# Kernel tuning notes

Hardware: AMD Instinct MI355X
Metric: run time of the kernel (lower is better)

The kernel has to match this reference:

```python
import jax, jax.numpy as jnp
import numpy as np

N_NODES = 100000
N_EDGES = 1600000
IN_CH, HID_CH, N_CLASS = 512, 128, 40


def setup_inputs() -> dict:
    key = jax.random.key(0)
    k1, k2, k3, k4 = jax.random.split(key, 4)
    x = jax.random.normal(k1, (N_NODES, IN_CH), dtype=jnp.float32)
    edge_index = jax.random.randint(k2, (2, N_EDGES), 0, N_NODES, dtype=jnp.int64)
    W1 = jax.random.normal(k3, (IN_CH, HID_CH), dtype=jnp.float32) * (1.0 / np.sqrt(IN_CH))
    b1 = jnp.zeros((HID_CH,), dtype=jnp.float32)
    W2 = jax.random.normal(k4, (HID_CH, N_CLASS), dtype=jnp.float32) * (1.0 / np.sqrt(HID_CH))
    b2 = jnp.zeros((N_CLASS,), dtype=jnp.float32)
    return {"x": x, "edge_index": edge_index, "W1": W1, "b1": b1, "W2": W2, "b2": b2}


def _gcn_conv(x, src, dst, norm, W, b, n_nodes):
    # transform then sparse normalized aggregation: out = D^-1/2 (A+I) D^-1/2 (x W) + b
    h = x @ W                                  # [N, out_ch]
    msg = h[src] * norm[:, None]               # gather + scale, [E+N, out_ch]
    return jax.ops.segment_sum(msg, dst, num_segments=n_nodes) + b


def reference(x, edge_index, W1, b1, W2, b2):
    n = x.shape[0]
    loop = jnp.arange(n, dtype=edge_index.dtype)
    src = jnp.concatenate([edge_index[0], loop])   # add self-loops
    dst = jnp.concatenate([edge_index[1], loop])
    deg = jax.ops.segment_sum(jnp.ones_like(src, dtype=x.dtype), dst, num_segments=n)
    dinv = jnp.where(deg > 0, jax.lax.rsqrt(deg), 0.0)
    norm = dinv[src] * dinv[dst]                   # symmetric normalization

    h = jax.nn.relu(_gcn_conv(x, src, dst, norm, W1, b1, n))
    # dropout(p=0.5, train=False) -> identity in eval mode
    logits = _gcn_conv(h, src, dst, norm, W2, b2, n)
    return jax.nn.log_softmax(logits, axis=1)
```

## Files before the change

### kernel.cpp

```cpp
#include <hip/hip_runtime.h>
#include <math.h>

#define IN_CH 512
#define HID 128
#define NCLASS 40
#define SCAN_CHUNK 2048
#define FILL_CHUNKS 2048

typedef __attribute__((ext_vector_type(8))) short short8;
typedef __attribute__((ext_vector_type(4))) float float4v;

static __device__ inline ushort f2bf(float f) {
    unsigned int u = __float_as_uint(f);
    u += 0x7fffu + ((u >> 16) & 1u);
    return (ushort)(u >> 16);
}
static __device__ inline float bf2f(ushort u) {
    return __uint_as_float(((unsigned int)u) << 16);
}

__global__ void k_count(const int* __restrict__ dst, int E, int* __restrict__ cnt) {
    int i = blockIdx.x * blockDim.x + threadIdx.x;
    if (i < E) atomicAdd(&cnt[dst[i]], 1);
}

__global__ void k_dinv(const int* __restrict__ cnt, float* __restrict__ dinv, int n) {
    int i = blockIdx.x * blockDim.x + threadIdx.x;
    if (i < n) dinv[i] = rsqrtf((float)cnt[i] + 1.0f);
}

__global__ __launch_bounds__(256) void k_scan_local(const int* __restrict__ cnt,
                                                    int* __restrict__ rowptr,
                                                    int* __restrict__ blocksum, int n) {
    __shared__ int ssum[256];
    int b = blockIdx.x, t = threadIdx.x;
    int base = b * SCAN_CHUNK + t * 8;
    int v[8], s = 0;
    #pragma unroll
    for (int i = 0; i < 8; ++i) {
        int idx = base + i;
        v[i] = (idx < n) ? cnt[idx] : 0;
        s += v[i];
    }
    ssum[t] = s;
    __syncthreads();
    for (int off = 1; off < 256; off <<= 1) {
        int x = (t >= off) ? ssum[t - off] : 0;
        __syncthreads();
        ssum[t] += x;
        __syncthreads();
    }
    int run = ssum[t] - s;
    #pragma unroll
    for (int i = 0; i < 8; ++i) {
        int idx = base + i;
        if (idx < n) rowptr[idx] = run;
        run += v[i];
    }
    if (t == 255) blocksum[b] = ssum[255];
}

__global__ void k_scan_blocksums(int* blocksum, int nb) {
    if (threadIdx.x == 0 && blockIdx.x == 0) {
        int acc = 0;
        for (int i = 0; i < nb; ++i) { int v = blocksum[i]; blocksum[i] = acc; acc += v; }
    }
}

__global__ void k_scan_add(int* __restrict__ rowptr, int* __restrict__ cursor,
                           const int* __restrict__ blocksum, int n) {
    int i = blockIdx.x * blockDim.x + threadIdx.x;
    if (i < n) {
        int r = rowptr[i] + blocksum[i / SCAN_CHUNK];
        rowptr[i] = r;
        cursor[i] = r;
    }
}

__global__ __launch_bounds__(256) void k_fill(const int* __restrict__ src,
                                              const int* __restrict__ dst,
                                              int* __restrict__ cursor,
                                              int* __restrict__ col, int E, int N) {
    int range = blockIdx.x & 7;
    int chunk = blockIdx.x >> 3;
    int r0 = (N >> 3) * range;
    int r1 = (range == 7) ? N : r0 + (N >> 3);
    int e0 = (int)((long long)E * chunk / FILL_CHUNKS);
    int e1 = (int)((long long)E * (chunk + 1) / FILL_CHUNKS);
    for (int e = e0 + threadIdx.x; e < e1; e += 256) {
        int d = dst[e];
        if (d >= r0 && d < r1) {
            int p = atomicAdd(&cursor[d], 1);
            col[p] = src[e];
        }
    }
}

__global__ void k_w1t(const float* __restrict__ W1, ushort* __restrict__ W1t) {
    int i = blockIdx.x * blockDim.x + threadIdx.x;
    int n = i >> 9;
    int k = i & 511;
    W1t[i] = f2bf(W1[k * HID + n]);
}

__global__ void k_w2t(const float* __restrict__ W2, ushort* __restrict__ W2t) {
    int i = blockIdx.x * blockDim.x + threadIdx.x;
    int n = i >> 7;
    int k = i & 127;
    float v = (n < NCLASS) ? W2[k * NCLASS + n] : 0.f;
    W2t[i] = f2bf(v);
}

#define GBM 128
#define GBK 64
#define KP 72
__global__ __launch_bounds__(256) void k_gemm1_mfma(const float* __restrict__ X,
                                                    const ushort* __restrict__ W1t,
                                                    const float* __restrict__ dinv,
                                                    ushort* __restrict__ H, int M) {
    __shared__ ushort As[GBM * KP];
    int t = threadIdx.x;
    int bm = blockIdx.x * GBM;
    int wave = t >> 6;
    int lane = t & 63;
    int m0w = (wave >> 1) * 64;
    int n0w = (wave & 1) * 64;
    int lrow = lane & 15;
    int quad = lane >> 4;

    float4v acc[4][4];
    #pragma unroll
    for (int i = 0; i < 4; ++i)
        #pragma unroll
        for (int j = 0; j < 4; ++j) acc[i][j] = (float4v)(0.f);

    int ar = t >> 1;
    int ah = (t & 1) * 32;
    int gmr = bm + ar;
    if (gmr >= M) gmr = M - 1;
    const float* gA = &X[(size_t)gmr * IN_CH + ah];

    float4 pre[8];
    #pragma unroll
    for (int i = 0; i < 8; ++i) pre[i] = *(const float4*)(gA + i * 4);

    for (int k0 = 0; k0 < IN_CH; k0 += GBK) {
        #pragma unroll
        for (int i = 0; i < 4; ++i) {
            union { ushort u[8]; uint4 v; } pk;
            float4 f0 = pre[2 * i], f1 = pre[2 * i + 1];
            pk.u[0] = f2bf(f0.x); pk.u[1] = f2bf(f0.y);
            pk.u[2] = f2bf(f0.z); pk.u[3] = f2bf(f0.w);
            pk.u[4] = f2bf(f1.x); pk.u[5] = f2bf(f1.y);
            pk.u[6] = f2bf(f1.z); pk.u[7] = f2bf(f1.w);
            *(uint4*)&As[ar * KP + ah + i * 8] = pk.v;
        }
        if (k0 + GBK < IN_CH) {
            #pragma unroll
            for (int i = 0; i < 8; ++i)
                pre[i] = *(const float4*)(gA + k0 + GBK + i * 4);
        }
        __syncthreads();
        #pragma unroll
        for (int kk = 0; kk < GBK; kk += 32) {
            short8 af[4], bfr[4];
            #pragma unroll
            for (int j = 0; j < 4; ++j)
                bfr[j] = *(const short8*)&W1t[(size_t)(n0w + j * 16 + lrow) * IN_CH
                                              + k0 + kk + quad * 8];
            #pragma unroll
            for (int i = 0; i < 4; ++i)
                af[i] = *(const short8*)&As[(m0w + i * 16 + lrow) * KP + kk + quad * 8];
            #pragma unroll
            for (int i = 0; i < 4; ++i)
                #pragma unroll
                for (int j = 0; j < 4; ++j)
                    acc[i][j] = __builtin_amdgcn_mfma_f32_16x16x32_bf16(
                        af[i], bfr[j], acc[i][j], 0, 0, 0);
        }
        __syncthreads();
    }
    #pragma unroll
    for (int i = 0; i < 4; ++i) {
        #pragma unroll
        for (int r = 0; r < 4; ++r) {
            int gm = bm + m0w + i * 16 + quad * 4 + r;
            if (gm < M) {
                float di = dinv[gm];
                #pragma unroll
                for (int j = 0; j < 4; ++j)
                    H[(size_t)gm * HID + n0w + j * 16 + lrow] = f2bf(acc[i][j][r] * di);
            }
        }
    }
}

__global__ __launch_bounds__(256) void k_agg1(const int* __restrict__ rowptr,
                                              const int* __restrict__ rowend,
                                              const int* __restrict__ col,
                                              const float* __restrict__ dinv,
                                              const unsigned int* __restrict__ h1b,
                                              const float* __restrict__ b1,
                                              unsigned int* __restrict__ hb, int N) {
    int wv = threadIdx.x >> 6;
    int t  = threadIdx.x & 63;
    int m = blockIdx.x * 4 + wv;
    if (m >= N) m = N - 1;
    float dm = dinv[m];
    unsigned int sv = h1b[(size_t)m * 64 + t];
    float ax = bf2f((ushort)(sv & 0xffff));
    float ay = bf2f((ushort)(sv >> 16));
    float bx = 0.f, by = 0.f;
    int j = rowptr[m], jend = rowend[m];
    for (; j + 8 <= jend; j += 8) {
        int s0 = col[j],     s1 = col[j + 1], s2 = col[j + 2], s3 = col[j + 3];
        int s4 = col[j + 4], s5 = col[j + 5], s6 = col[j + 6], s7 = col[j + 7];
        unsigned int v0 = h1b[(size_t)s0 * 64 + t];
        unsigned int v1 = h1b[(size_t)s1 * 64 + t];
        unsigned int v2 = h1b[(size_t)s2 * 64 + t];
        unsigned int v3 = h1b[(size_t)s3 * 64 + t];
        unsigned int v4 = h1b[(size_t)s4 * 64 + t];
        unsigned int v5 = h1b[(size_t)s5 * 64 + t];
        unsigned int v6 = h1b[(size_t)s6 * 64 + t];
        unsigned int v7 = h1b[(size_t)s7 * 64 + t];
        ax += bf2f((ushort)(v0 & 0xffff)); ay += bf2f((ushort)(v0 >> 16));
        bx += bf2f((ushort)(v1 & 0xffff)); by += bf2f((ushort)(v1 >> 16));
        ax += bf2f((ushort)(v2 & 0xffff)); ay += bf2f((ushort)(v2 >> 16));
        bx += bf2f((ushort)(v3 & 0xffff)); by += bf2f((ushort)(v3 >> 16));
        ax += bf2f((ushort)(v4 & 0xffff)); ay += bf2f((ushort)(v4 >> 16));
        bx += bf2f((ushort)(v5 & 0xffff)); by += bf2f((ushort)(v5 >> 16));
        ax += bf2f((ushort)(v6 & 0xffff)); ay += bf2f((ushort)(v6 >> 16));
        bx += bf2f((ushort)(v7 & 0xffff)); by += bf2f((ushort)(v7 >> 16));
    }
    for (; j + 4 <= jend; j += 4) {
        int s0 = col[j], s1 = col[j + 1], s2 = col[j + 2], s3 = col[j + 3];
        unsigned int v0 = h1b[(size_t)s0 * 64 + t];
        unsigned int v1 = h1b[(size_t)s1 * 64 + t];
        unsigned int v2 = h1b[(size_t)s2 * 64 + t];
        unsigned int v3 = h1b[(size_t)s3 * 64 + t];
        ax += bf2f((ushort)(v0 & 0xffff)); ay += bf2f((ushort)(v0 >> 16));
        bx += bf2f((ushort)(v1 & 0xffff)); by += bf2f((ushort)(v1 >> 16));
        ax += bf2f((ushort)(v2 & 0xffff)); ay += bf2f((ushort)(v2 >> 16));
        bx += bf2f((ushort)(v3 & 0xffff)); by += bf2f((ushort)(v3 >> 16));
    }
    for (; j < jend; ++j) {
        int s = col[j];
        unsigned int v = h1b[(size_t)s * 64 + t];
        ax += bf2f((ushort)(v & 0xffff)); ay += bf2f((ushort)(v >> 16));
    }
    ax += bx; ay += by;
    float2 bb = ((const float2*)b1)[t];
    float hx = fmaxf(fmaf(ax, dm, bb.x), 0.f);
    float hy = fmaxf(fmaf(ay, dm, bb.y), 0.f);
    hx *= dm;
    hy *= dm;
    hb[(size_t)m * 64 + t] = (unsigned int)f2bf(hx) | ((unsigned int)f2bf(hy) << 16);
}

__global__ __launch_bounds__(256) void k_gemm2_mfma(const ushort* __restrict__ hb,
                                                    const ushort* __restrict__ W2t,
                                                    ushort* __restrict__ h2s, int M) {
    int t = threadIdx.x;
    int wave = t >> 6, lane = t & 63;
    int lrow = lane & 15, quad = lane >> 4;
    int row0 = blockIdx.x * 64 + wave * 16;
    int rm = row0 + lrow;
    if (rm >= M) rm = M - 1;
    const ushort* pa = &hb[(size_t)rm * HID + quad * 8];
    float4v acc[3];
    acc[0] = (float4v)(0.f); acc[1] = (float4v)(0.f); acc[2] = (float4v)(0.f);
    #pragma unroll
    for (int k0 = 0; k0 < HID; k0 += 32) {
        short8 a = *(const short8*)(pa + k0);
        #pragma unroll
        for (int jj = 0; jj < 3; ++jj) {
            short8 b = *(const short8*)&W2t[(size_t)(jj * 16 + lrow) * HID
                                            + k0 + quad * 8];
            acc[jj] = __builtin_amdgcn_mfma_f32_16x16x32_bf16(a, b, acc[jj], 0, 0, 0);
        }
    }
    #pragma unroll
    for (int jj = 0; jj < 3; ++jj) {
        int cls = jj * 16 + lrow;
        #pragma unroll
        for (int r = 0; r < 4; ++r) {
            int node = row0 + quad * 4 + r;
            if (node < M && cls < NCLASS)
                h2s[(size_t)node * NCLASS + cls] = f2bf(acc[jj][r]);
        }
    }
}

__global__ __launch_bounds__(256) void k_agg2_final(const int* __restrict__ rowptr,
                                                    const int* __restrict__ rowend,
                                                    const int* __restrict__ col,
                                                    const float* __restrict__ dinv,
                                                    const unsigned int* __restrict__ h2p,
                                                    const float* __restrict__ b2,
                                                    float* __restrict__ out, int N) {
    int wv = threadIdx.x >> 6;
    int t  = threadIdx.x & 63;
    int m = blockIdx.x * 4 + wv;
    if (m >= N) m = N - 1;
    float dm = dinv[m];
    int g = (t >= 40) ? 2 : ((t >= 20) ? 1 : 0);
    int u = t - g * 20;
    bool act = t < 60;
    float vx = 0.f, vy = 0.f;
    if (t < 20) {
        unsigned int v = h2p[(size_t)m * 20 + u];
        vx = bf2f((ushort)(v & 0xffff));
        vy = bf2f((ushort)(v >> 16));
    }
    int j = rowptr[m] + g, jend = rowend[m];
    if (act) {
        for (; j + 3 < jend; j += 6) {
            int s0 = col[j], s1 = col[j + 3];
            unsigned int v0 = h2p[(size_t)s0 * 20 + u];
            unsigned int v1 = h2p[(size_t)s1 * 20 + u];
            vx += bf2f((ushort)(v0 & 0xffff)); vy += bf2f((ushort)(v0 >> 16));
            vx += bf2f((ushort)(v1 & 0xffff)); vy += bf2f((ushort)(v1 >> 16));
        }
        if (j < jend) {
            int s = col[j];
            unsigned int v = h2p[(size_t)s * 20 + u];
            vx += bf2f((ushort)(v & 0xffff)); vy += bf2f((ushort)(v >> 16));
        }
    }
    vx += __shfl(vx, t + 20) + __shfl(vx, t + 40);
    vy += __shfl(vy, t + 20) + __shfl(vy, t + 40);
    bool w = t < 20;
    float lx = 0.f, ly = 0.f;
    if (w) {
        float2 bb = ((const float2*)b2)[u];
        lx = fmaf(vx, dm, bb.x);
        ly = fmaf(vy, dm, bb.y);
    }
    float mv = w ? fmaxf(lx, ly) : -INFINITY;
    #pragma unroll
    for (int off = 32; off; off >>= 1) mv = fmaxf(mv, __shfl_xor(mv, off));
    float ex = w ? (expf(lx - mv) + expf(ly - mv)) : 0.f;
    #pragma unroll
    for (int off = 32; off; off >>= 1) ex += __shfl_xor(ex, off);
    float lse = mv + logf(ex);
    if (w) ((float2*)out)[(size_t)m * 20 + u] = make_float2(lx - lse, ly - lse);
}

extern "C" void kernel_launch(void* const* d_in, const int* in_sizes, int n_in,
                              void* d_out, int out_size, void* d_ws, size_t ws_size,
                              hipStream_t stream) {
    const float* x  = (const float*)d_in[0];
    const int*   ei = (const int*)d_in[1];
    const float* W1 = (const float*)d_in[2];
    const float* b1 = (const float*)d_in[3];
    const float* W2 = (const float*)d_in[4];
    const float* b2 = (const float*)d_in[5];
    float* out = (float*)d_out;

    const int N = in_sizes[0] / IN_CH;
    const int E = in_sizes[1] / 2;
    const int* src = ei;
    const int* dst = ei + E;

    const int NB_SCAN = (N + SCAN_CHUNK - 1) / SCAN_CHUNK;

    size_t Npad = ((size_t)N + 127) / 128 * 128;
    float* ws = (float*)d_ws;
    float* dinv    = ws;
    int*   cnt     = (int*)(ws + Npad);
    int*   rowptr  = (int*)(ws + 2 * Npad);
    int*   cursor  = (int*)(ws + 3 * Npad);
    int*   bsum    = (int*)(ws + 4 * Npad);
    int*   col     = (int*)(ws + 4 * Npad + 128);
    size_t o_h1    = 4 * Npad + 128 + (size_t)E;
    unsigned int* h1b = (unsigned int*)(ws + o_h1);
    unsigned int* hb  = (unsigned int*)(ws + o_h1 + (size_t)N * 64);
    unsigned int* h2p = (unsigned int*)(ws + o_h1 + (size_t)N * 128);
    ushort* W2t = (ushort*)(ws + o_h1 + (size_t)N * 148);
    ushort* W1t = (ushort*)h2p;

    hipMemsetAsync(cnt, 0, (size_t)N * sizeof(int), stream);
    k_count<<<(E + 255) / 256, 256, 0, stream>>>(dst, E, cnt);
    k_dinv<<<(N + 255) / 256, 256, 0, stream>>>(cnt, dinv, N);
    k_scan_local<<<NB_SCAN, 256, 0, stream>>>(cnt, rowptr, bsum, N);
    k_scan_blocksums<<<1, 64, 0, stream>>>(bsum, NB_SCAN);
    k_scan_add<<<(N + 255) / 256, 256, 0, stream>>>(rowptr, cursor, bsum, N);
    k_fill<<<8 * FILL_CHUNKS, 256, 0, stream>>>(src, dst, cursor, col, E, N);

    k_w1t<<<(HID * IN_CH) / 256, 256, 0, stream>>>(W1, W1t);
    k_w2t<<<24, 256, 0, stream>>>(W2, W2t);
    k_gemm1_mfma<<<(N + GBM - 1) / GBM, 256, 0, stream>>>(x, W1t, dinv,
                                                          (ushort*)h1b, N);
    k_agg1<<<(N + 3) / 4, 256, 0, stream>>>(rowptr, cursor, col, dinv,
                                            h1b, b1, hb, N);

    k_gemm2_mfma<<<(N + 63) / 64, 256, 0, stream>>>((const ushort*)hb, W2t,
                                                    (ushort*)h2p, N);
    k_agg2_final<<<(N + 3) / 4, 256, 0, stream>>>(rowptr, cursor, col, dinv,
                                                  h2p, b2, out, N);
}
```

Before: 616.7 us.

## Fuse setup kernels, restructure CSR fill, vectorize layer-1 gather with half-wave edges

Folds the dinv computation into the scan-add kernel and merges the two weight-transpose kernels, cutting the launch count. The CSR fill now launches one block per edge chunk: each thread loads four edges once and loops over the eight destination ranges, instead of eight blocks each re-reading the same edges. The layer-1 aggregation has each half-wave take alternate edges with 8-byte loads, then combines the halves with a cross-half shuffle, so each neighbour fetch is a wider access and more edges are in flight. Cheaper bf16 unpack helpers replace the mask-and-shift conversions, at the cost of a changed order of atomics and of float additions.

```diff
diff --git a/kernel.cpp b/kernel.cpp
--- a/kernel.cpp
+++ b/kernel.cpp
@@ -18,15 +18,12 @@
 static __device__ inline float bf2f(ushort u) {
     return __uint_as_float(((unsigned int)u) << 16);
 }
+static __device__ inline float blo(unsigned int u) { return __uint_as_float(u << 16); }
+static __device__ inline float bhi(unsigned int u) { return __uint_as_float(u & 0xffff0000u); }
 
 __global__ void k_count(const int* __restrict__ dst, int E, int* __restrict__ cnt) {
     int i = blockIdx.x * blockDim.x + threadIdx.x;
     if (i < E) atomicAdd(&cnt[dst[i]], 1);
-}
-
-__global__ void k_dinv(const int* __restrict__ cnt, float* __restrict__ dinv, int n) {
-    int i = blockIdx.x * blockDim.x + threadIdx.x;
-    if (i < n) dinv[i] = rsqrtf((float)cnt[i] + 1.0f);
 }
 
 __global__ __launch_bounds__(256) void k_scan_local(const int* __restrict__ cnt,
@@ -67,13 +64,16 @@
     }
 }
 
-__global__ void k_scan_add(int* __restrict__ rowptr, int* __restrict__ cursor,
-                           const int* __restrict__ blocksum, int n) {
+__global__ void k_scan_add_dinv(int* __restrict__ rowptr, int* __restrict__ cursor,
+                                const int* __restrict__ blocksum,
+                                const int* __restrict__ cnt,
+                                float* __restrict__ dinv, int n) {
     int i = blockIdx.x * blockDim.x + threadIdx.x;
     if (i < n) {
         int r = rowptr[i] + blocksum[i / SCAN_CHUNK];
         rowptr[i] = r;
         cursor[i] = r;
+        dinv[i] = rsqrtf((float)cnt[i] + 1.0f);
     }
 }
 
@@ -81,34 +81,40 @@
                                               const int* __restrict__ dst,
                                               int* __restrict__ cursor,
                                               int* __restrict__ col, int E, int N) {
-    int range = blockIdx.x & 7;
-    int chunk = blockIdx.x >> 3;
-    int r0 = (N >> 3) * range;
-    int r1 = (range == 7) ? N : r0 + (N >> 3);
+    int chunk = blockIdx.x;
     int e0 = (int)((long long)E * chunk / FILL_CHUNKS);
     int e1 = (int)((long long)E * (chunk + 1) / FILL_CHUNKS);
-    for (int e = e0 + threadIdx.x; e < e1; e += 256) {
-        int d = dst[e];
-        if (d >= r0 && d < r1) {
-            int p = atomicAdd(&cursor[d], 1);
-            col[p] = src[e];
-        }
-    }
-}
-
-__global__ void k_w1t(const float* __restrict__ W1, ushort* __restrict__ W1t) {
+    int e = e0 + threadIdx.x;
+    int s0 = 0, d0 = -1, s1 = 0, d1 = -1, s2 = 0, d2 = -1, s3 = 0, d3 = -1;
+    if (e < e1)       { s0 = src[e];       d0 = dst[e]; }
+    if (e + 256 < e1) { s1 = src[e + 256]; d1 = dst[e + 256]; }
+    if (e + 512 < e1) { s2 = src[e + 512]; d2 = dst[e + 512]; }
+    if (e + 768 < e1) { s3 = src[e + 768]; d3 = dst[e + 768]; }
+    #pragma unroll
+    for (int r = 0; r < 8; ++r) {
+        int r0 = (N >> 3) * r;
+        int r1 = (r == 7) ? N : r0 + (N >> 3);
+        if (d0 >= r0 && d0 < r1) { int p = atomicAdd(&cursor[d0], 1); col[p] = s0; }
+        if (d1 >= r0 && d1 < r1) { int p = atomicAdd(&cursor[d1], 1); col[p] = s1; }
+        if (d2 >= r0 && d2 < r1) { int p = atomicAdd(&cursor[d2], 1); col[p] = s2; }
+        if (d3 >= r0 && d3 < r1) { int p = atomicAdd(&cursor[d3], 1); col[p] = s3; }
+    }
+}
+
+__global__ void k_wt(const float* __restrict__ W1, const float* __restrict__ W2,
+                     ushort* __restrict__ W1t, ushort* __restrict__ W2t) {
     int i = blockIdx.x * blockDim.x + threadIdx.x;
-    int n = i >> 9;
-    int k = i & 511;
-    W1t[i] = f2bf(W1[k * HID + n]);
-}
-
-__global__ void k_w2t(const float* __restrict__ W2, ushort* __restrict__ W2t) {
-    int i = blockIdx.x * blockDim.x + threadIdx.x;
-    int n = i >> 7;
-    int k = i & 127;
-    float v = (n < NCLASS) ? W2[k * NCLASS + n] : 0.f;
-    W2t[i] = f2bf(v);
+    if (i < HID * IN_CH) {
+        int n = i >> 9;
+        int k = i & 511;
+        W1t[i] = f2bf(W1[k * HID + n]);
+    } else {
+        int q = i - HID * IN_CH;
+        int n = q >> 7;
+        int k = q & 127;
+        float v = (n < NCLASS) ? W2[k * NCLASS + n] : 0.f;
+        W2t[q] = f2bf(v);
+    }
 }
 
 #define GBM 128
@@ -204,57 +210,56 @@
                                               unsigned int* __restrict__ hb, int N) {
     int wv = threadIdx.x >> 6;
     int t  = threadIdx.x & 63;
+    int half = t >> 5;
+    int l    = t & 31;
     int m = blockIdx.x * 4 + wv;
     if (m >= N) m = N - 1;
     float dm = dinv[m];
-    unsigned int sv = h1b[(size_t)m * 64 + t];
-    float ax = bf2f((ushort)(sv & 0xffff));
-    float ay = bf2f((ushort)(sv >> 16));
-    float bx = 0.f, by = 0.f;
+    float c0 = 0.f, c1 = 0.f, c2 = 0.f, c3 = 0.f;
+    if (half == 0) {
+        uint2 sv = *(const uint2*)&h1b[(size_t)m * 64 + 2 * l];
+        c0 = blo(sv.x); c1 = bhi(sv.x); c2 = blo(sv.y); c3 = bhi(sv.y);
+    }
     int j = rowptr[m], jend = rowend[m];
     for (; j + 8 <= jend; j += 8) {
-        int s0 = col[j],     s1 = col[j + 1], s2 = col[j + 2], s3 = col[j + 3];
-        int s4 = col[j + 4], s5 = col[j + 5], s6 = col[j + 6], s7 = col[j + 7];
-        unsigned int v0 = h1b[(size_t)s0 * 64 + t];
-        unsigned int v1 = h1b[(size_t)s1 * 64 + t];
-        unsigned int v2 = h1b[(size_t)s2 * 64 + t];
-        unsigned int v3 = h1b[(size_t)s3 * 64 + t];
-        unsigned int v4 = h1b[(size_t)s4 * 64 + t];
-        unsigned int v5 = h1b[(size_t)s5 * 64 + t];
-        unsigned int v6 = h1b[(size_t)s6 * 64 + t];
-        unsigned int v7 = h1b[(size_t)s7 * 64 + t];
-        ax += bf2f((ushort)(v0 & 0xffff)); ay += bf2f((ushort)(v0 >> 16));
-        bx += bf2f((ushort)(v1 & 0xffff)); by += bf2f((ushort)(v1 >> 16));
-        ax += bf2f((ushort)(v2 & 0xffff)); ay += bf2f((ushort)(v2 >> 16));
-        bx += bf2f((ushort)(v3 & 0xffff)); by += bf2f((ushort)(v3 >> 16));
-        ax += bf2f((ushort)(v4 & 0xffff)); ay += bf2f((ushort)(v4 >> 16));
-        bx += bf2f((ushort)(v5 & 0xffff)); by += bf2f((ushort)(v5 >> 16));
-        ax += bf2f((ushort)(v6 & 0xffff)); ay += bf2f((ushort)(v6 >> 16));
-        bx += bf2f((ushort)(v7 & 0xffff)); by += bf2f((ushort)(v7 >> 16));
-    }
-    for (; j + 4 <= jend; j += 4) {
-        int s0 = col[j], s1 = col[j + 1], s2 = col[j + 2], s3 = col[j + 3];
-        unsigned int v0 = h1b[(size_t)s0 * 64 + t];
-        unsigned int v1 = h1b[(size_t)s1 * 64 + t];
-        unsigned int v2 = h1b[(size_t)s2 * 64 + t];
-        unsigned int v3 = h1b[(size_t)s3 * 64 + t];
-        ax += bf2f((ushort)(v0 & 0xffff)); ay += bf2f((ushort)(v0 >> 16));
-        bx += bf2f((ushort)(v1 & 0xffff)); by += bf2f((ushort)(v1 >> 16));
-        ax += bf2f((ushort)(v2 & 0xffff)); ay += bf2f((ushort)(v2 >> 16));
-        bx += bf2f((ushort)(v3 & 0xffff)); by += bf2f((ushort)(v3 >> 16));
-    }
-    for (; j < jend; ++j) {
+        int sA = col[j + 0 + half];
+        int sB = col[j + 2 + half];
+        int sC = col[j + 4 + half];
+        int sD = col[j + 6 + half];
+        uint2 vA = *(const uint2*)&h1b[(size_t)sA * 64 + 2 * l];
+        uint2 vB = *(const uint2*)&h1b[(size_t)sB * 64 + 2 * l];
+        uint2 vC = *(const uint2*)&h1b[(size_t)sC * 64 + 2 * l];
+        uint2 vD = *(const uint2*)&h1b[(size_t)sD * 64 + 2 * l];
+        c0 += blo(vA.x); c1 += bhi(vA.x); c2 += blo(vA.y); c3 += bhi(vA.y);
+        c0 += blo(vB.x); c1 += bhi(vB.x); c2 += blo(vB.y); c3 += bhi(vB.y);
+        c0 += blo(vC.x); c1 += bhi(vC.x); c2 += blo(vC.y); c3 += bhi(vC.y);
+        c0 += blo(vD.x); c1 += bhi(vD.x); c2 += blo(vD.y); c3 += bhi(vD.y);
+    }
+    for (; j + 2 <= jend; j += 2) {
+        int s = col[j + half];
+        uint2 v = *(const uint2*)&h1b[(size_t)s * 64 + 2 * l];
+        c0 += blo(v.x); c1 += bhi(v.x); c2 += blo(v.y); c3 += bhi(v.y);
+    }
+    if (j < jend && half == 0) {
         int s = col[j];
-        unsigned int v = h1b[(size_t)s * 64 + t];
-        ax += bf2f((ushort)(v & 0xffff)); ay += bf2f((ushort)(v >> 16));
-    }
-    ax += bx; ay += by;
-    float2 bb = ((const float2*)b1)[t];
-    float hx = fmaxf(fmaf(ax, dm, bb.x), 0.f);
-    float hy = fmaxf(fmaf(ay, dm, bb.y), 0.f);
-    hx *= dm;
-    hy *= dm;
-    hb[(size_t)m * 64 + t] = (unsigned int)f2bf(hx) | ((unsigned int)f2bf(hy) << 16);
+        uint2 v = *(const uint2*)&h1b[(size_t)s * 64 + 2 * l];
+        c0 += blo(v.x); c1 += bhi(v.x); c2 += blo(v.y); c3 += bhi(v.y);
+    }
+    c0 += __shfl_xor(c0, 32);
+    c1 += __shfl_xor(c1, 32);
+    c2 += __shfl_xor(c2, 32);
+    c3 += __shfl_xor(c3, 32);
+    if (half == 0) {
+        float4 bb = *(const float4*)&b1[4 * l];
+        float h0 = fmaxf(fmaf(c0, dm, bb.x), 0.f) * dm;
+        float h1 = fmaxf(fmaf(c1, dm, bb.y), 0.f) * dm;
+        float h2 = fmaxf(fmaf(c2, dm, bb.z), 0.f) * dm;
+        float h3 = fmaxf(fmaf(c3, dm, bb.w), 0.f) * dm;
+        uint2 o;
+        o.x = (unsigned int)f2bf(h0) | ((unsigned int)f2bf(h1) << 16);
+        o.y = (unsigned int)f2bf(h2) | ((unsigned int)f2bf(h3) << 16);
+        *(uint2*)&hb[(size_t)m * 64 + 2 * l] = o;
+    }
 }
 
 __global__ __launch_bounds__(256) void k_gemm2_mfma(const ushort* __restrict__ hb,
@@ -309,8 +314,8 @@
     float vx = 0.f, vy = 0.f;
     if (t < 20) {
         unsigned int v = h2p[(size_t)m * 20 + u];
-        vx = bf2f((ushort)(v & 0xffff));
-        vy = bf2f((ushort)(v >> 16));
+        vx = blo(v);
+        vy = bhi(v);
     }
     int j = rowptr[m] + g, jend = rowend[m];
     if (act) {
@@ -318,13 +323,13 @@
             int s0 = col[j], s1 = col[j + 3];
             unsigned int v0 = h2p[(size_t)s0 * 20 + u];
             unsigned int v1 = h2p[(size_t)s1 * 20 + u];
-            vx += bf2f((ushort)(v0 & 0xffff)); vy += bf2f((ushort)(v0 >> 16));
-            vx += bf2f((ushort)(v1 & 0xffff)); vy += bf2f((ushort)(v1 >> 16));
+            vx += blo(v0); vy += bhi(v0);
+            vx += blo(v1); vy += bhi(v1);
         }
         if (j < jend) {
             int s = col[j];
             unsigned int v = h2p[(size_t)s * 20 + u];
-            vx += bf2f((ushort)(v & 0xffff)); vy += bf2f((ushort)(v >> 16));
+            vx += blo(v); vy += bhi(v);
         }
     }
     vx += __shfl(vx, t + 20) + __shfl(vx, t + 40);
@@ -381,14 +386,13 @@
 
     hipMemsetAsync(cnt, 0, (size_t)N * sizeof(int), stream);
     k_count<<<(E + 255) / 256, 256, 0, stream>>>(dst, E, cnt);
-    k_dinv<<<(N + 255) / 256, 256, 0, stream>>>(cnt, dinv, N);
     k_scan_local<<<NB_SCAN, 256, 0, stream>>>(cnt, rowptr, bsum, N);
     k_scan_blocksums<<<1, 64, 0, stream>>>(bsum, NB_SCAN);
-    k_scan_add<<<(N + 255) / 256, 256, 0, stream>>>(rowptr, cursor, bsum, N);
-    k_fill<<<8 * FILL_CHUNKS, 256, 0, stream>>>(src, dst, cursor, col, E, N);
-
-    k_w1t<<<(HID * IN_CH) / 256, 256, 0, stream>>>(W1, W1t);
-    k_w2t<<<24, 256, 0, stream>>>(W2, W2t);
+    k_scan_add_dinv<<<(N + 255) / 256, 256, 0, stream>>>(rowptr, cursor, bsum,
+                                                         cnt, dinv, N);
+    k_fill<<<FILL_CHUNKS, 256, 0, stream>>>(src, dst, cursor, col, E, N);
+
+    k_wt<<<(HID * IN_CH + 48 * HID) / 256, 256, 0, stream>>>(W1, W2, W1t, W2t);
     k_gemm1_mfma<<<(N + GBM - 1) / GBM, 256, 0, stream>>>(x, W1t, dinv,
                                                           (ushort*)h1b, N);
     k_agg1<<<(N + 3) / 4, 256, 0, stream>>>(rowptr, cursor, col, dinv,
```

Measured after the change: 643.6 us. +4.4%, slower.
